# Optimization experiments

Hardware: AMD Instinct MI355X
Metric: run time of the kernel (lower is better)

## Reference

```python
import jax, jax.numpy as jnp
import numpy as np


def setup_inputs() -> dict:
    key = jax.random.key(0)
    ks = jax.random.split(key, 6)
    B, n_tok, n_RoI = 8, 64, 100
    T_hidden, I_hidden = 768, 1024
    P = I_hidden // 2  # projection = 512
    s_q = 1.0 / np.sqrt(T_hidden)
    s_k = 1.0 / np.sqrt(I_hidden)
    s_w = 1.0 / np.sqrt(P)
    return {
        "encT": jax.random.normal(ks[0], (B, n_tok, T_hidden), jnp.float32),
        "encI": jax.random.normal(ks[1], (B, n_RoI, I_hidden), jnp.float32),
        "mask": jnp.zeros((B, 1, n_tok, n_RoI), jnp.float32),
        "Wq": jax.random.normal(ks[2], (T_hidden, P), jnp.float32) * s_q,
        "bq": jnp.zeros((P,), jnp.float32),
        "Wk": jax.random.normal(ks[3], (I_hidden, P), jnp.float32) * s_k,
        "bk": jnp.zeros((P,), jnp.float32),
        "w": jax.random.normal(ks[4], (P,), jnp.float32) * s_w,
        "b": jnp.zeros((1,), jnp.float32),
    }


def reference(encT, encI, mask, Wq, bq, Wk, bk, w, b):
    # Q_mlp / K_mlp: Linear + exact GELU (torch nn.GELU default)
    q = jax.nn.gelu(jnp.einsum('bth,hp->btp', encT, Wq) + bq, approximate=False)  # [B,T,P]
    k = jax.nn.gelu(jnp.einsum('brh,hp->brp', encI, Wk) + bk, approximate=False)  # [B,R,P]
    # broadcast add (instead of repeat/view), tanh, then Linear(P,1)
    fusion = jnp.tanh(q[:, :, None, :] + k[:, None, :, :])  # [B,T,R,P]
    logits = jnp.einsum('btrp,p->btr', fusion, w) + b[0]      # [B,T,R]
    return logits + jnp.squeeze(mask, axis=1)
```

## Files before the change

kernel.cpp:

```cpp
#include <hip/hip_runtime.h>
#include <hip/hip_fp16.h>
#include <math.h>

#define B_  8
#define T_  64
#define R_  100
#define TH_ 768
#define IH_ 1024
#define P_  512
#define N_  512

#define CTANH 2.88539008177792681f

typedef short short8  __attribute__((ext_vector_type(8)));
typedef float floatx4 __attribute__((ext_vector_type(4)));

__device__ __forceinline__ ushort f2bf(float f) {
  union { float f; unsigned int u; } v; v.f = f;
  unsigned int r = v.u + 0x7FFFu + ((v.u >> 16) & 1u);
  return (ushort)(r >> 16);
}

#define PADK 40

__global__ __launch_bounds__(1024) void mfma_linear_gelu_sk4(
    const float* __restrict__ encT, const float* __restrict__ Wq,
    const float* __restrict__ bq, __half* __restrict__ qout,
    const float* __restrict__ encI, const float* __restrict__ Wk,
    const float* __restrict__ bk, __half* __restrict__ kout) {
  const int rt = blockIdx.y;
  const bool isQ = rt < 8;
  const float* __restrict__ X = isQ ? encT : encI;
  const float* __restrict__ W = isQ ? Wq : Wk;
  const float* __restrict__ bias = isQ ? bq : bk;
  __half* __restrict__ Y = isQ ? qout : kout;
  const int M    = isQ ? (B_ * T_) : (B_ * R_);
  const int KDIM = isQ ? TH_ : IH_;
  const int row0 = (isQ ? rt : (rt - 8)) * 64;
  const int col0 = blockIdx.x * 32;
  const int kq   = KDIM >> 2;
  const int ntiles = kq / 32;

  __shared__ ushort As[4][64 * PADK];
  __shared__ ushort Bs[4][32 * PADK];
  __shared__ float  red[2][64 * 33];

  const int tid = threadIdx.x;
  const int sp  = tid >> 8;
  const int t   = tid & 255;
  const int kbase = sp * kq;

  const int arow = t >> 2;
  const int akq  = (t & 3) * 8;
  const int arowc = min(row0 + arow, M - 1);
  const float* __restrict__ Xp = X + (size_t)arowc * KDIM + kbase + akq;

  const int bkp = (t >> 4) * 2;
  const int bn2 = (t & 15) * 2;
  const float* __restrict__ Wp = W + (size_t)(kbase + bkp) * N_ + col0 + bn2;

  const int wv = t >> 6;
  const int lane = t & 63;
  const int wm = wv * 16;
  const int l15 = lane & 15;
  const int q8  = (lane >> 4) * 8;
  const int q4  = (lane >> 4) * 4;

  floatx4 acc0 = {0.f,0.f,0.f,0.f}, acc1 = {0.f,0.f,0.f,0.f};

  float4 a0 = *(const float4*)(Xp);
  float4 a1 = *(const float4*)(Xp + 4);
  float2 b0 = *(const float2*)(Wp);
  float2 b1 = *(const float2*)(Wp + N_);

  for (int kt = 0; kt < ntiles; ++kt) {
    {
      short8 pk;
      pk[0] = (short)f2bf(a0.x); pk[1] = (short)f2bf(a0.y);
      pk[2] = (short)f2bf(a0.z); pk[3] = (short)f2bf(a0.w);
      pk[4] = (short)f2bf(a1.x); pk[5] = (short)f2bf(a1.y);
      pk[6] = (short)f2bf(a1.z); pk[7] = (short)f2bf(a1.w);
      *(short8*)&As[sp][arow * PADK + akq] = pk;
    }
    {
      unsigned int p0 = (unsigned int)f2bf(b0.x) | ((unsigned int)f2bf(b1.x) << 16);
      unsigned int p1 = (unsigned int)f2bf(b0.y) | ((unsigned int)f2bf(b1.y) << 16);
      *(unsigned int*)&Bs[sp][(bn2 + 0) * PADK + bkp] = p0;
      *(unsigned int*)&Bs[sp][(bn2 + 1) * PADK + bkp] = p1;
    }
    __syncthreads();

    if (kt + 1 < ntiles) {
      const int kb = (kt + 1) * 32;
      a0 = *(const float4*)(Xp + kb);
      a1 = *(const float4*)(Xp + kb + 4);
      b0 = *(const float2*)(Wp + (size_t)kb * N_);
      b1 = *(const float2*)(Wp + (size_t)(kb + 1) * N_);
    }

    short8 af  = *(const short8*)&As[sp][(wm + l15) * PADK + q8];
    short8 bf0 = *(const short8*)&Bs[sp][(l15) * PADK + q8];
    short8 bf1 = *(const short8*)&Bs[sp][(16 + l15) * PADK + q8];
    acc0 = __builtin_amdgcn_mfma_f32_16x16x32_bf16(af, bf0, acc0, 0, 0, 0);
    acc1 = __builtin_amdgcn_mfma_f32_16x16x32_bf16(af, bf1, acc1, 0, 0, 0);
    __syncthreads();
  }

  if (sp >= 2) {
    float* L = red[sp - 2];
    #pragma unroll
    for (int j = 0; j < 4; ++j) {
      L[(wm + q4 + j) * 33 + l15]      = acc0[j];
      L[(wm + q4 + j) * 33 + 16 + l15] = acc1[j];
    }
  }
  __syncthreads();
  if (sp < 2) {
    const float* L = red[sp];
    #pragma unroll
    for (int j = 0; j < 4; ++j) {
      acc0[j] += L[(wm + q4 + j) * 33 + l15];
      acc1[j] += L[(wm + q4 + j) * 33 + 16 + l15];
    }
  }
  __syncthreads();
  if (sp == 1) {
    float* L = red[0];
    #pragma unroll
    for (int j = 0; j < 4; ++j) {
      L[(wm + q4 + j) * 33 + l15]      = acc0[j];
      L[(wm + q4 + j) * 33 + 16 + l15] = acc1[j];
    }
  }
  __syncthreads();
  if (sp == 0) {
    const float* L = red[0];
    const float is2 = 0.70710678118654752f;
    const float bia0 = bias[col0 + l15];
    const float bia1 = bias[col0 + 16 + l15];
    #pragma unroll
    for (int j = 0; j < 4; ++j) {
      const int row = row0 + wm + q4 + j;
      if (row < M) {
        float v0 = acc0[j] + L[(wm + q4 + j) * 33 + l15] + bia0;
        float v1 = acc1[j] + L[(wm + q4 + j) * 33 + 16 + l15] + bia1;
        v0 = CTANH * 0.5f * v0 * (1.f + erff(v0 * is2));
        v1 = CTANH * 0.5f * v1 * (1.f + erff(v1 * is2));
        Y[(size_t)row * N_ + col0 + l15]      = __float2half(v0);
        Y[(size_t)row * N_ + col0 + 16 + l15] = __float2half(v1);
      }
    }
  }
}

__global__ __launch_bounds__(256) void fuse_kernel_h(
    const __half* __restrict__ q, const __half* __restrict__ k,
    const float* __restrict__ w, const float* __restrict__ bscalar,
    const float* __restrict__ mask, float* __restrict__ out) {
  const int bt = blockIdx.x;
  const int wave = threadIdx.x >> 6;
  const int rg = blockIdx.y * 4 + wave;
  if (rg >= 25) return;
  const int lane = threadIdx.x & 63;
  const int sub  = lane >> 4;
  const int pi   = lane & 15;
  const int r = rg * 4 + sub;
  const int b = bt >> 6;

  const __half* __restrict__ qp = q + (size_t)bt * P_ + pi * 8;
  const __half* __restrict__ kp = k + (size_t)(b * R_ + r) * P_ + pi * 8;
  const float* __restrict__ wp = w + pi * 8;

  float acc0 = 0.f, acc1 = 0.f;
  #pragma unroll
  for (int i = 0; i < 4; ++i) {
    union { float4 f; __half2 h[4]; } qu, ku;
    qu.f = *(const float4*)(qp + i * 128);
    ku.f = *(const float4*)(kp + i * 128);
    float4 w0 = *(const float4*)(wp + i * 128);
    float4 w1 = *(const float4*)(wp + i * 128 + 4);
    #pragma unroll
    for (int e = 0; e < 4; ++e) {
      __half2 s = __hadd2(qu.h[e], ku.h[e]);
      float x0 = __low2float(s);
      float x1 = __high2float(s);
      float d0 = __builtin_amdgcn_rcpf(1.f + __builtin_amdgcn_exp2f(x0));
      float d1 = __builtin_amdgcn_rcpf(1.f + __builtin_amdgcn_exp2f(x1));
      float s0 = fmaf(-2.f, d0, 1.f);
      float s1 = fmaf(-2.f, d1, 1.f);
      const float we0 = (e == 0) ? w0.x : (e == 1) ? w0.z : (e == 2) ? w1.x : w1.z;
      const float we1 = (e == 0) ? w0.y : (e == 1) ? w0.w : (e == 2) ? w1.y : w1.w;
      acc0 = fmaf(we0, s0, acc0);
      acc1 = fmaf(we1, s1, acc1);
    }
  }
  float acc = acc0 + acc1;
  #pragma unroll
  for (int off = 1; off < 16; off <<= 1) acc += __shfl_xor(acc, off, 64);

  if (pi == 0) {
    out[(size_t)bt * R_ + r] = acc + bscalar[0] + mask[(size_t)bt * R_ + r];
  }
}

extern "C" void kernel_launch(void* const* d_in, const int* in_sizes, int n_in,
                              void* d_out, int out_size, void* d_ws, size_t ws_size,
                              hipStream_t stream) {
  const float* encT = (const float*)d_in[0];
  const float* encI = (const float*)d_in[1];
  const float* mask = (const float*)d_in[2];
  const float* Wq   = (const float*)d_in[3];
  const float* bq   = (const float*)d_in[4];
  const float* Wk   = (const float*)d_in[5];
  const float* bk   = (const float*)d_in[6];
  const float* w    = (const float*)d_in[7];
  const float* bsc  = (const float*)d_in[8];
  float* out = (float*)d_out;

  __half* q = (__half*)d_ws;
  __half* k = q + (size_t)B_ * T_ * P_;

  dim3 grid(N_ / 32, 8 + 13);
  mfma_linear_gelu_sk4<<<grid, 1024, 0, stream>>>(encT, Wq, bq, q,
                                                  encI, Wk, bk, k);

  fuse_kernel_h<<<dim3(512, 7), 256, 0, stream>>>(q, k, w, bsc, mask, out);
}
```

Measured before the change: 96.38 us.

## Factor tanh exponent into per-operand exp so fusion uses product instead of exp

```diff
diff --git a/kernel.cpp b/kernel.cpp
--- a/kernel.cpp
+++ b/kernel.cpp
@@ -23,11 +23,13 @@
 
 #define PADK 40
 
-__global__ __launch_bounds__(1024) void mfma_linear_gelu_sk4(
+__global__ __launch_bounds__(1024) void mfma_linear_gelu_exp_sk4(
     const float* __restrict__ encT, const float* __restrict__ Wq,
     const float* __restrict__ bq, __half* __restrict__ qout,
     const float* __restrict__ encI, const float* __restrict__ Wk,
-    const float* __restrict__ bk, __half* __restrict__ kout) {
+    const float* __restrict__ bk, __half* __restrict__ kout,
+    const float* __restrict__ wvec, const float* __restrict__ bscalar,
+    float* __restrict__ swb) {
   const int rt = blockIdx.y;
   const bool isQ = rt < 8;
   const float* __restrict__ X = isQ ? encT : encI;
@@ -144,18 +146,28 @@
       if (row < M) {
         float v0 = acc0[j] + L[(wm + q4 + j) * 33 + l15] + bia0;
         float v1 = acc1[j] + L[(wm + q4 + j) * 33 + 16 + l15] + bia1;
-        v0 = CTANH * 0.5f * v0 * (1.f + erff(v0 * is2));
-        v1 = CTANH * 0.5f * v1 * (1.f + erff(v1 * is2));
-        Y[(size_t)row * N_ + col0 + l15]      = __float2half(v0);
-        Y[(size_t)row * N_ + col0 + 16 + l15] = __float2half(v1);
+        v0 = 0.5f * v0 * (1.f + erff(v0 * is2));
+        v1 = 0.5f * v1 * (1.f + erff(v1 * is2));
+        Y[(size_t)row * N_ + col0 + l15]      = __float2half(__builtin_amdgcn_exp2f(CTANH * v0));
+        Y[(size_t)row * N_ + col0 + 16 + l15] = __float2half(__builtin_amdgcn_exp2f(CTANH * v1));
       }
     }
   }
-}
-
-__global__ __launch_bounds__(256) void fuse_kernel_h(
+
+  if (blockIdx.x == 0 && blockIdx.y == 0 && tid < 64) {
+    float s = 0.f;
+    const float* wp = wvec + tid * 8;
+    #pragma unroll
+    for (int j = 0; j < 8; ++j) s += wp[j];
+    #pragma unroll
+    for (int off = 1; off < 64; off <<= 1) s += __shfl_xor(s, off, 64);
+    if (tid == 0) swb[0] = s + bscalar[0];
+  }
+}
+
+__global__ __launch_bounds__(256) void fuse_kernel_exp(
     const __half* __restrict__ q, const __half* __restrict__ k,
-    const float* __restrict__ w, const float* __restrict__ bscalar,
+    const float* __restrict__ w, const float* __restrict__ swb,
     const float* __restrict__ mask, float* __restrict__ out) {
   const int bt = blockIdx.x;
   const int wave = threadIdx.x >> 6;
@@ -181,17 +193,15 @@
     float4 w1 = *(const float4*)(wp + i * 128 + 4);
     #pragma unroll
     for (int e = 0; e < 4; ++e) {
-      __half2 s = __hadd2(qu.h[e], ku.h[e]);
-      float x0 = __low2float(s);
-      float x1 = __high2float(s);
-      float d0 = __builtin_amdgcn_rcpf(1.f + __builtin_amdgcn_exp2f(x0));
-      float d1 = __builtin_amdgcn_rcpf(1.f + __builtin_amdgcn_exp2f(x1));
-      float s0 = fmaf(-2.f, d0, 1.f);
-      float s1 = fmaf(-2.f, d1, 1.f);
+      __half2 m = __hmul2(qu.h[e], ku.h[e]);
+      float x0 = __low2float(m);
+      float x1 = __high2float(m);
+      float d0 = __builtin_amdgcn_rcpf(x0 + 1.f);
+      float d1 = __builtin_amdgcn_rcpf(x1 + 1.f);
       const float we0 = (e == 0) ? w0.x : (e == 1) ? w0.z : (e == 2) ? w1.x : w1.z;
       const float we1 = (e == 0) ? w0.y : (e == 1) ? w0.w : (e == 2) ? w1.y : w1.w;
-      acc0 = fmaf(we0, s0, acc0);
-      acc1 = fmaf(we1, s1, acc1);
+      acc0 = fmaf(we0, d0, acc0);
+      acc1 = fmaf(we1, d1, acc1);
     }
   }
   float acc = acc0 + acc1;
@@ -199,7 +209,7 @@
   for (int off = 1; off < 16; off <<= 1) acc += __shfl_xor(acc, off, 64);
 
   if (pi == 0) {
-    out[(size_t)bt * R_ + r] = acc + bscalar[0] + mask[(size_t)bt * R_ + r];
+    out[(size_t)bt * R_ + r] = fmaf(-2.f, acc, swb[0]) + mask[(size_t)bt * R_ + r];
   }
 }
 
@@ -219,10 +229,12 @@
 
   __half* q = (__half*)d_ws;
   __half* k = q + (size_t)B_ * T_ * P_;
+  float* swb = (float*)(k + (size_t)B_ * R_ * P_);
 
   dim3 grid(N_ / 32, 8 + 13);
-  mfma_linear_gelu_sk4<<<grid, 1024, 0, stream>>>(encT, Wq, bq, q,
-                                                  encI, Wk, bk, k);
-
-  fuse_kernel_h<<<dim3(512, 7), 256, 0, stream>>>(q, k, w, bsc, mask, out);
-}
+  mfma_linear_gelu_exp_sk4<<<grid, 1024, 0, stream>>>(encT, Wq, bq, q,
+                                                      encI, Wk, bk, k,
+                                                      w, bsc, swb);
+
+  fuse_kernel_exp<<<dim3(512, 7), 256, 0, stream>>>(q, k, w, swb, mask, out);
+}
```

After: 94.16 us. 2.3% less time.
